# Kernel optimization log

Measured on AMD Instinct MI355X. Metric: run time of the kernel, lower is better.

The kernel has to match this reference:

```python
import jax, jax.numpy as jnp
import numpy as np

B, C, H, W = 128, 1280, 16, 16


def _conv1x1(x, w, b):
    # 1x1 conv == per-pixel linear over channels: (O,C) x (B,C,H,W) -> (B,O,H,W)
    return jnp.einsum('oc,bchw->bohw', w, x) + b[None, :, None, None]


def setup_inputs() -> dict:
    key = jax.random.key(0)
    ks = jax.random.split(key, 10)
    s = 1.0 / np.sqrt(C)
    inp = {
        'x': jax.random.normal(ks[0], (B, C, H, W), dtype=jnp.float32),
        'Wk': jax.random.uniform(ks[1], (C, C), jnp.float32, -s, s),
        'bk': jax.random.uniform(ks[2], (C,), jnp.float32, -s, s),
        'Wq': jax.random.uniform(ks[3], (C, C), jnp.float32, -s, s),
        'bq': jax.random.uniform(ks[4], (C,), jnp.float32, -s, s),
        'Wv': jax.random.uniform(ks[5], (C, C), jnp.float32, -s, s),
        'bv': jax.random.uniform(ks[6], (C,), jnp.float32, -s, s),
        'Wr': jax.random.uniform(ks[7], (C, C), jnp.float32, -s, s),
        'br': jax.random.uniform(ks[8], (C,), jnp.float32, -s, s),
        'alpha': 0.1 * jax.random.normal(ks[9], (1,), dtype=jnp.float32),
    }
    return inp


def reference(x, Wk, bk, Wq, bq, Wv, bv, Wr, br, alpha):
    b, c, h, w = x.shape
    hw = h * w
    k = _conv1x1(x, Wk, bk).reshape(b, c, hw)   # (B,C,HW)
    q = _conv1x1(x, Wq, bq).reshape(b, c, hw)   # (B,C,HW)
    v = _conv1x1(x, Wv, bv).reshape(b, c, hw)   # (B,C,HW)
    # K^T Q: (B,HW,HW) == keys.view.permute(0,2,1) @ queries.view
    scores = jnp.einsum('bcn,bcm->bnm', k, q)
    # torch.nn.Softmax2d on a 3D tensor applies softmax over dim=-3 (here: batch)
    attn = jax.nn.softmax(scores, axis=0)
    # attn @ V^T: (B,HW,HW) @ (B,HW,C) -> (B,HW,C)
    att = jnp.einsum('bnm,bmc->bnc', attn, v.transpose(0, 2, 1))
    att = att.transpose(0, 2, 1).reshape(b, c, h, w)
    out = _conv1x1(att, Wr, br)
    return alpha * out + x
```

## Files before the change

### kernel.cpp

```cpp
#include <hip/hip_runtime.h>
#include <hip/hip_bf16.h>

typedef __attribute__((ext_vector_type(8))) short bf16x8;
typedef __attribute__((ext_vector_type(4))) float f32x4;

#define GLD16(g, s) __builtin_amdgcn_global_load_lds( \
    (const __attribute__((address_space(1))) void*)(g), \
    (__attribute__((address_space(3))) void*)(s), 16, 0, 0)

#define SBAR() __builtin_amdgcn_sched_barrier(0)
#define WAIT_LGKM(n) do { asm volatile("s_waitcnt lgkmcnt(" #n ")" ::: "memory"); SBAR(); } while (0)

static constexpr int kB  = 128;
static constexpr int kC  = 1280;
static constexpr int kHW = 256;

__device__ __forceinline__ float bf2f(unsigned short u) {
    return __uint_as_float(((unsigned int)u) << 16);
}

template<int OUT_MODE, int BIAS_MODE, int ORDER>
__device__ __forceinline__ void gemm_body(
    const __hip_bfloat16* __restrict__ A,
    const __hip_bfloat16* __restrict__ Bt,
    void* __restrict__ outp,
    const float* __restrict__ bias,
    const float* __restrict__ resid,
    const float* __restrict__ alphap,
    const float* __restrict__ aux1,
    const float* __restrict__ aux2,
    int M, int N, int K,
    int ldA, int ldB, long sA, long sB, long sC, int ldC,
    char* smem, int z)
{
    const int t = threadIdx.x;
    const int w = t >> 6, l = t & 63;
    const int q = l >> 4, r16 = l & 15;
    const int wr = w >> 2, wc = w & 3;
    const int nbm = M >> 8, nbn = N >> 8;
    const int nwg = nbm * nbn;
    int f = blockIdx.x;
    {
        const int q8 = nwg >> 3, r8 = nwg & 7;
        const int xcd = f & 7, rank = f >> 3;
        f = (xcd < r8 ? xcd * (q8 + 1) : r8 * (q8 + 1) + (xcd - r8) * q8) + rank;
    }
    long m0, n0;
    if (ORDER == 0) { m0 = (long)(f % nbm) << 8; n0 = (long)(f / nbm) << 8; }
    else            { n0 = (long)(f % nbn) << 8; m0 = (long)(f / nbn) << 8; }
    const char* Azb = (const char*)(A + (long)z * sA);
    const char* Bzb = (const char*)(Bt + (long)z * sB);

    const char* pa[4];
    const char* pb[4];
    int ldsd[4];
    #pragma unroll
    for (int i = 0; i < 4; ++i) {
        const int d = i * 8192 + t * 16;
        const int row = d >> 7;
        const int cb = (d & 127) ^ ((row & 7) << 4);
        pa[i] = Azb + ((m0 + row) * (long)ldA) * 2 + cb;
        pb[i] = Bzb + ((n0 + row) * (long)ldB) * 2 + cb;
        ldsd[i] = d;
    }
    auto stage = [&](int slot) {
        char* base = smem + slot * 65536;
        #pragma unroll
        for (int i = 0; i < 4; ++i) GLD16(pa[i], base + ldsd[i]);
        #pragma unroll
        for (int i = 0; i < 4; ++i) GLD16(pb[i], base + 32768 + ldsd[i]);
        #pragma unroll
        for (int i = 0; i < 4; ++i) { pa[i] += 128; pb[i] += 128; }
    };

    const int mask = (l & 7) << 4;
    const int cx  = (q << 4) ^ mask;
    int offA[2], offB[2];
    offA[0] = (wr * 128 + r16) * 128 + cx;
    offA[1] = (wr * 128 + r16) * 128 + (cx ^ 64);
    offB[0] = 32768 + (wc * 64 + r16) * 128 + cx;
    offB[1] = 32768 + (wc * 64 + r16) * 128 + (cx ^ 64);

#define DSA(dst, bs_, mih, kk) do { const char* p_ = (bs_) + offA[kk] + (mih) * 8192; \
    dst[0] = *(const bf16x8*)(p_);        dst[1] = *(const bf16x8*)(p_ + 2048); \
    dst[2] = *(const bf16x8*)(p_ + 4096); dst[3] = *(const bf16x8*)(p_ + 6144); } while (0)
#define DSB(dst, bs_, kk) do { const char* p_ = (bs_) + offB[kk]; \
    dst[0] = *(const bf16x8*)(p_);        dst[1] = *(const bf16x8*)(p_ + 2048); \
    dst[2] = *(const bf16x8*)(p_ + 4096); dst[3] = *(const bf16x8*)(p_ + 6144); } while (0)
#define MM16(ar, br, mih) do { __builtin_amdgcn_s_setprio(1); \
    _Pragma("unroll") for (int j = 0; j < 4; ++j) \
    _Pragma("unroll") for (int ni = 0; ni < 4; ++ni) \
        acc[(mih) * 4 + j][ni] = __builtin_amdgcn_mfma_f32_16x16x32_bf16( \
            ar[j], br[ni], acc[(mih) * 4 + j][ni], 0, 0, 0); \
    __builtin_amdgcn_s_setprio(0); SBAR(); } while (0)

    f32x4 acc[8][4] = {};
    const int nK = K >> 6;
    stage(0);

    for (int tk = 0; tk < nK; ++tk) {
        const int s = tk & 1;
        asm volatile("s_waitcnt vmcnt(0)" ::: "memory");
        SBAR();
        __builtin_amdgcn_s_barrier();
        SBAR();
        if (tk + 1 < nK) stage(s ^ 1);
        SBAR();

        const char* bs_ = smem + s * 65536;
        bf16x8 aP[4], bP[4], aQ[4], bQ[4];
        DSB(bP, bs_, 0); DSA(aP, bs_, 0, 0);
        DSA(aQ, bs_, 1, 0);
        WAIT_LGKM(4);  MM16(aP, bP, 0);
        DSB(bQ, bs_, 1); DSA(aP, bs_, 0, 1);
        WAIT_LGKM(8);  MM16(aQ, bP, 1);
        DSA(aQ, bs_, 1, 1);
        WAIT_LGKM(4);  MM16(aP, bQ, 0);
        WAIT_LGKM(0);  MM16(aQ, bQ, 1);
        asm volatile("s_waitcnt lgkmcnt(0)" ::: "memory");
        SBAR();
        __builtin_amdgcn_s_barrier();
        SBAR();
    }

    const float alpha = (OUT_MODE >= 3) ? alphap[0] : 0.0f;
    #pragma unroll
    for (int mi = 0; mi < 8; ++mi) {
        #pragma unroll
        for (int ni = 0; ni < 4; ++ni) {
            #pragma unroll
            for (int r = 0; r < 4; ++r) {
                const long row = m0 + wr * 128 + mi * 16 + q * 4 + r;
                const long col = n0 + wc * 64 + ni * 16 + r16;
                float vv = acc[mi][ni][r];
                if (BIAS_MODE == 1) vv += bias[col];
                if (BIAS_MODE == 2) vv += bias[row];
                if (OUT_MODE == 0) {
                    ((__hip_bfloat16*)outp)[(long)z * sC + row * ldC + col] = __float2bfloat16(vv);
                } else if (OUT_MODE == 1) {
                    ((float*)outp)[(long)z * sC + row * ldC + col] = vv;
                } else if (OUT_MODE == 2) {
                    const long addr = (col >> 8) * (long)(kC * kHW) + row * kHW + (col & 255);
                    ((__hip_bfloat16*)outp)[addr] = __float2bfloat16(vv);
                } else if (OUT_MODE == 3) {
                    const long addr = (col >> 8) * (long)(kC * kHW) + row * kHW + (col & 255);
                    ((float*)outp)[addr] = alpha * vv + resid[addr];
                } else {
                    const long addr = (long)z * (kC * kHW) + row * kHW + col;
                    const float term = vv + aux1[row] * aux2[(long)z * 256 + col] + bias[row];
                    ((float*)outp)[addr] = alpha * term + resid[addr];
                }
            }
        }
    }
#undef DSA
#undef DSB
#undef MM16
}

template<int OUT_MODE, int BIAS_MODE, int ORDER>
__global__ __launch_bounds__(512, 2) void gemm_q(
    const __hip_bfloat16* __restrict__ A,
    const __hip_bfloat16* __restrict__ Bt,
    void* __restrict__ outp,
    const float* __restrict__ bias,
    const float* __restrict__ resid,
    const float* __restrict__ alphap,
    const float* __restrict__ aux1,
    const float* __restrict__ aux2,
    int M, int N, int K,
    int ldA, int ldB, long sA, long sB, long sC, int ldC)
{
    extern __shared__ char smem[];
    gemm_body<OUT_MODE, BIAS_MODE, ORDER>(A, Bt, outp, bias, resid, alphap,
        aux1, aux2, M, N, K, ldA, ldB, sA, sB, sC, ldC, smem, blockIdx.z);
}

__global__ __launch_bounds__(512, 2) void gemm_dual(
    const __hip_bfloat16* __restrict__ xT,
    const __hip_bfloat16* __restrict__ G,
    __hip_bfloat16* __restrict__ uT,
    const float* __restrict__ w1,
    const __hip_bfloat16* __restrict__ W2,
    __hip_bfloat16* __restrict__ rv)
{
    extern __shared__ char smem[];
    if (blockIdx.z == 0) {
        gemm_body<0, 1, 1>(xT, G, uT, w1, nullptr, nullptr, nullptr, nullptr,
            32768, 1280, 1280, 1280, 1280, 0, 0, 0, 1280, smem, 0);
    } else {
        gemm_body<2, 0, 0>(W2, xT, rv, nullptr, nullptr, nullptr, nullptr, nullptr,
            1280, 32768, 1280, 1280, 1280, 0, 0, 0, 0, smem, 0);
    }
}

__global__ __launch_bounds__(512, 2) void gemm_gsplit(
    const __hip_bfloat16* __restrict__ WkT,
    const __hip_bfloat16* __restrict__ WqT,
    const __hip_bfloat16* __restrict__ Wrb,
    const __hip_bfloat16* __restrict__ WvT,
    float* __restrict__ Gp)
{
    extern __shared__ char smem[];
    const int zz = blockIdx.z;
    const int pair = zz >> 1, ks = zz & 1;
    const __hip_bfloat16* A  = (pair ? Wrb : WkT) + ks * 640;
    const __hip_bfloat16* Bt = (pair ? WvT : WqT) + ks * 640;
    gemm_body<1, 0, 0>(A, Bt, Gp, nullptr, nullptr, nullptr, nullptr, nullptr,
        1280, 1280, 640, 1280, 1280, 0, 0, 1638400, 1280, smem, zz);
}

__global__ __launch_bounds__(256) void reduce_gw(
    const float* __restrict__ Gp,
    __hip_bfloat16* __restrict__ G, __hip_bfloat16* __restrict__ W2)
{
    const long i = ((long)blockIdx.x * 256 + threadIdx.x) * 4;
    const float4 a = *reinterpret_cast<const float4*>(Gp + i);
    const float4 b = *reinterpret_cast<const float4*>(Gp + 1638400 + i);
    G[i + 0] = __float2bfloat16(a.x + b.x);
    G[i + 1] = __float2bfloat16(a.y + b.y);
    G[i + 2] = __float2bfloat16(a.z + b.z);
    G[i + 3] = __float2bfloat16(a.w + b.w);
    const float4 c = *reinterpret_cast<const float4*>(Gp + 2L * 1638400 + i);
    const float4 d = *reinterpret_cast<const float4*>(Gp + 3L * 1638400 + i);
    W2[i + 0] = __float2bfloat16(c.x + d.x);
    W2[i + 1] = __float2bfloat16(c.y + d.y);
    W2[i + 2] = __float2bfloat16(c.z + d.z);
    W2[i + 3] = __float2bfloat16(c.w + d.w);
}

__global__ __launch_bounds__(256) void transpose_x(
    const float* __restrict__ x, __hip_bfloat16* __restrict__ xT,
    const float* __restrict__ w2, float* __restrict__ c2s)
{
    __shared__ float tile[64][65];
    __shared__ float red[4][64];
    const int b = blockIdx.z;
    const int c0 = blockIdx.x * 64;
    const int p0 = blockIdx.y * 64;
    const int tj = threadIdx.x & 63;
    const int ti = threadIdx.x >> 6;
    const float* xb = x + ((long)b * kC + c0) * kHW + p0;
    #pragma unroll
    for (int i = 0; i < 16; ++i) {
        const int c = i * 4 + ti;
        tile[c][tj] = xb[(long)c * kHW + tj];
    }
    __syncthreads();
    __hip_bfloat16* o = xT + ((long)(b * kHW + p0)) * kC + c0;
    #pragma unroll
    for (int i = 0; i < 16; ++i) {
        const int p = i * 4 + ti;
        o[(long)p * kC + tj] = __float2bfloat16(tile[tj][p]);
    }
    float s = 0.0f;
    #pragma unroll
    for (int j = 0; j < 16; ++j)
        s += tile[ti * 16 + j][tj] * w2[c0 + ti * 16 + j];
    red[ti][tj] = s;
    __syncthreads();
    if (ti == 0)
        atomicAdd(&c2s[b * 256 + p0 + tj], red[0][tj] + red[1][tj] + red[2][tj] + red[3][tj]);
}

__global__ __launch_bounds__(256) void transpose_w4(
    const float* __restrict__ Wk, __hip_bfloat16* __restrict__ WkT,
    const float* __restrict__ Wq, __hip_bfloat16* __restrict__ WqT,
    const float* __restrict__ Wv, __hip_bfloat16* __restrict__ WvT,
    const float* __restrict__ Wr, __hip_bfloat16* __restrict__ Wrb)
{
    const int zz = blockIdx.z;
    const float* W = (zz == 0) ? Wk : (zz == 1) ? Wq : (zz == 2) ? Wv : Wr;
    __hip_bfloat16* WT = (zz == 0) ? WkT : (zz == 1) ? WqT : (zz == 2) ? WvT : Wrb;
    __shared__ float tile[64][65];
    const int o0 = blockIdx.x * 64;
    const int c0 = blockIdx.y * 64;
    const int tj = threadIdx.x & 63;
    const int ti = threadIdx.x >> 6;
    #pragma unroll
    for (int i = 0; i < 16; ++i) {
        const int o = i * 4 + ti;
        tile[o][tj] = W[(long)(o0 + o) * kC + c0 + tj];
    }
    __syncthreads();
    if (zz < 3) {
        #pragma unroll
        for (int i = 0; i < 16; ++i) {
            const int c = i * 4 + ti;
            WT[(long)(c0 + c) * kC + o0 + tj] = __float2bfloat16(tile[tj][c]);
        }
    } else {
        #pragma unroll
        for (int i = 0; i < 16; ++i) {
            const int o = i * 4 + ti;
            WT[(long)(o0 + o) * kC + c0 + tj] = __float2bfloat16(tile[o][tj]);
        }
    }
}

__global__ __launch_bounds__(256) void zero_f32(float* __restrict__ p)
{
    reinterpret_cast<float4*>(p)[blockIdx.x * 256 + threadIdx.x] =
        make_float4(0.f, 0.f, 0.f, 0.f);
}

__global__ __launch_bounds__(256) void gemv_col(
    const float* __restrict__ Wk, const float* __restrict__ bq,
    const float* __restrict__ Wq, const float* __restrict__ bk,
    float* __restrict__ w1, float* __restrict__ w2)
{
    const float* W = blockIdx.y ? Wq : Wk;
    const float* v = blockIdx.y ? bk : bq;
    float* out = blockIdx.y ? w2 : w1;
    const int lj = threadIdx.x & 63;
    const int wid = threadIdx.x >> 6;
    const int c = blockIdx.x * 64 + lj;
    __shared__ float red[4][64];
    float s = 0.0f;
    for (int o = wid * 320; o < (wid + 1) * 320; ++o)
        s += W[(long)o * kC + c] * v[o];
    red[wid][lj] = s;
    __syncthreads();
    if (wid == 0) out[c] = red[0][lj] + red[1][lj] + red[2][lj] + red[3][lj];
}

__global__ __launch_bounds__(256) void gemv_row(
    const float* __restrict__ Wr, const float* __restrict__ bv, float* __restrict__ out)
{
    const int wid = threadIdx.x >> 6, lj = threadIdx.x & 63;
    const int o = blockIdx.x * 4 + wid;
    float s = 0.0f;
    #pragma unroll
    for (int j = 0; j < 20; ++j)
        s += Wr[(long)o * kC + j * 64 + lj] * bv[j * 64 + lj];
    #pragma unroll
    for (int off = 32; off > 0; off >>= 1) s += __shfl_down(s, off);
    if (lj == 0) out[o] = s;
}

__global__ __launch_bounds__(256) void dot_k(
    const float* __restrict__ a, const float* __restrict__ b, float* __restrict__ out)
{
    __shared__ float red[256];
    const int t_ = threadIdx.x;
    float s = 0.0f;
    for (int j = t_; j < kC; j += 256) s += a[j] * b[j];
    red[t_] = s; __syncthreads();
    for (int off = 128; off > 0; off >>= 1) {
        if (t_ < off) red[t_] += red[t_ + off];
        __syncthreads();
    }
    if (t_ == 0) out[0] = red[0];
}

__global__ __launch_bounds__(256) void rowsum_attn(
    const __hip_bfloat16* __restrict__ attn, float* __restrict__ rs)
{
    const int wid = threadIdx.x >> 6, lj = threadIdx.x & 63;
    const long p = (long)blockIdx.x * 4 + wid;
    const ushort4 v = *(const ushort4*)((const char*)attn + p * 512 + lj * 8);
    float s = bf2f(v.x) + bf2f(v.y) + bf2f(v.z) + bf2f(v.w);
    #pragma unroll
    for (int off = 32; off > 0; off >>= 1) s += __shfl_down(s, off);
    if (lj == 0) rs[p] = s;
}

__global__ __launch_bounds__(256) void softmax_batch(
    const float* __restrict__ sc, __hip_bfloat16* __restrict__ attn,
    const float* __restrict__ c2s, const float* __restrict__ c0p)
{
    const int pos = blockIdx.x * 256 + threadIdx.x;
    const int mcol = pos & 255;
    const float c0v = c0p[0];
    float m = -3.0e38f, s = 0.0f;
    for (int b = 0; b < kB; ++b) {
        const float v = sc[(long)b * 65536 + pos] + c2s[b * 256 + mcol] + c0v;
        const float mn = fmaxf(m, v);
        s = s * __expf(m - mn) + __expf(v - mn);
        m = mn;
    }
    const float rinv = 1.0f / s;
    for (int b = 0; b < kB; ++b) {
        const float v = sc[(long)b * 65536 + pos] + c2s[b * 256 + mcol] + c0v;
        attn[(long)b * 65536 + pos] = __float2bfloat16(__expf(v - m) * rinv);
    }
}

extern "C" void kernel_launch(void* const* d_in, const int* in_sizes, int n_in,
                              void* d_out, int out_size, void* d_ws, size_t ws_size,
                              hipStream_t stream)
{
    const float* x  = (const float*)d_in[0];
    const float* Wk = (const float*)d_in[1];
    const float* bk = (const float*)d_in[2];
    const float* Wq = (const float*)d_in[3];
    const float* bq = (const float*)d_in[4];
    const float* Wv = (const float*)d_in[5];
    const float* bv = (const float*)d_in[6];
    const float* Wr = (const float*)d_in[7];
    const float* br = (const float*)d_in[8];
    const float* al = (const float*)d_in[9];

    char* ws = (char*)d_ws;
    __hip_bfloat16* xT   = (__hip_bfloat16*)(ws);
    __hip_bfloat16* uT   = (__hip_bfloat16*)(ws + 83886080L);
    __hip_bfloat16* rv   = (__hip_bfloat16*)(ws + 167772160L);
    float*          sc   = (float*)(ws + 251658240L);
    __hip_bfloat16* attn = (__hip_bfloat16*)(ws + 285212672L);
    __hip_bfloat16* WkT  = (__hip_bfloat16*)(ws + 301989888L);
    __hip_bfloat16* Wrb  = (__hip_bfloat16*)(ws + 305266688L);
    __hip_bfloat16* WqT  = (__hip_bfloat16*)(ws + 308543488L);
    __hip_bfloat16* WvT  = (__hip_bfloat16*)(ws + 311820288L);
    __hip_bfloat16* G    = (__hip_bfloat16*)(ws + 315097088L);
    __hip_bfloat16* W2   = (__hip_bfloat16*)(ws + 318373888L);
    float*          w1   = (float*)(ws + 321650688L);
    float*          w2v  = (float*)(ws + 321655808L);
    float*          wrbv = (float*)(ws + 321660928L);
    float*          c0b  = (float*)(ws + 321666048L);
    float*          c2s  = (float*)(ws + 321666560L);
    float*          rs   = (float*)(ws + 321797632L);
    float*          Gp   = (float*)(ws + 321928704L);

    const int SMEM = 131072;
    hipFuncSetAttribute((const void*)gemm_q<1,0,0>, hipFuncAttributeMaxDynamicSharedMemorySize, SMEM);
    hipFuncSetAttribute((const void*)gemm_q<4,0,0>, hipFuncAttributeMaxDynamicSharedMemorySize, SMEM);
    hipFuncSetAttribute((const void*)gemm_dual,     hipFuncAttributeMaxDynamicSharedMemorySize, SMEM);
    hipFuncSetAttribute((const void*)gemm_gsplit,   hipFuncAttributeMaxDynamicSharedMemorySize, SMEM);

    transpose_w4<<<dim3(20, 20, 4), 256, 0, stream>>>(Wk, WkT, Wq, WqT, Wv, WvT, Wr, Wrb);
    gemv_col<<<dim3(20, 2), 256, 0, stream>>>(Wk, bq, Wq, bk, w1, w2v);
    gemv_row<<<320, 256, 0, stream>>>(Wr, bv, wrbv);
    dot_k<<<1, 256, 0, stream>>>(bk, bq, c0b);
    zero_f32<<<32, 256, 0, stream>>>(c2s);
    transpose_x<<<dim3(20, 4, 128), 256, 0, stream>>>(x, xT, w2v, c2s);

    gemm_gsplit<<<dim3(25, 1, 4), 512, SMEM, stream>>>(WkT, WqT, Wrb, WvT, Gp);
    reduce_gw<<<1600, 256, 0, stream>>>(Gp, G, W2);
    gemm_dual<<<dim3(640, 1, 2), 512, SMEM, stream>>>(xT, G, uT, w1, W2, rv);
    gemm_q<1, 0, 0><<<dim3(1, 1, 128), 512, SMEM, stream>>>(xT, uT, sc,
        nullptr, nullptr, nullptr, nullptr, nullptr,
        256, 256, 1280, 1280, 1280, 327680, 327680, 65536, 256);
    softmax_batch<<<256, 256, 0, stream>>>(sc, attn, c2s, c0b);
    rowsum_attn<<<8192, 256, 0, stream>>>(attn, rs);
    gemm_q<4, 0, 0><<<dim3(5, 1, 128), 512, SMEM, stream>>>(rv, attn, d_out,
        br, x, al, wrbv, rs,
        1280, 256, 256, 256, 256, 327680, 65536, 0, 0);
}
```

Baseline: 507.7 us.

## Split-K scores GEMM with atomics, deepen G split-K, merge small preprocessing kernels

The batched scores GEMM is split over K into two halves per batch, giving 256 blocks instead of 128, and accumulates into a pre-zeroed fp32 buffer with atomicAdd. The weight-product GEMM split-K goes from 2 to 4 slices, so it runs 200 blocks, and the reduction sums four partials. The tiny gemv and dot kernels are folded into one launch, and the zeroing of the scores buffer is combined with the c2s zeroing. This trades extra atomic traffic, a 32MB zero pass and a larger partial reduction for better CU occupancy and fewer launches. Gp now aliases the uT region, which is safe only because uT is written after reduce_gw consumes Gp.

```diff
diff --git a/kernel.cpp b/kernel.cpp
--- a/kernel.cpp
+++ b/kernel.cpp
@@ -145,10 +145,12 @@
                 } else if (OUT_MODE == 3) {
                     const long addr = (col >> 8) * (long)(kC * kHW) + row * kHW + (col & 255);
                     ((float*)outp)[addr] = alpha * vv + resid[addr];
-                } else {
+                } else if (OUT_MODE == 4) {
                     const long addr = (long)z * (kC * kHW) + row * kHW + col;
                     const float term = vv + aux1[row] * aux2[(long)z * 256 + col] + bias[row];
                     ((float*)outp)[addr] = alpha * term + resid[addr];
+                } else {
+                    atomicAdd(&((float*)outp)[(long)z * sC + row * ldC + col], vv);
                 }
             }
         }
@@ -203,11 +205,11 @@
 {
     extern __shared__ char smem[];
     const int zz = blockIdx.z;
-    const int pair = zz >> 1, ks = zz & 1;
-    const __hip_bfloat16* A  = (pair ? Wrb : WkT) + ks * 640;
-    const __hip_bfloat16* Bt = (pair ? WvT : WqT) + ks * 640;
+    const int pair = zz >> 2, kq = zz & 3;
+    const __hip_bfloat16* A  = (pair ? Wrb : WkT) + kq * 320;
+    const __hip_bfloat16* Bt = (pair ? WvT : WqT) + kq * 320;
     gemm_body<1, 0, 0>(A, Bt, Gp, nullptr, nullptr, nullptr, nullptr, nullptr,
-        1280, 1280, 640, 1280, 1280, 0, 0, 1638400, 1280, smem, zz);
+        1280, 1280, 320, 1280, 1280, 0, 0, 1638400, 1280, smem, zz);
 }
 
 __global__ __launch_bounds__(256) void reduce_gw(
@@ -215,18 +217,39 @@
     __hip_bfloat16* __restrict__ G, __hip_bfloat16* __restrict__ W2)
 {
     const long i = ((long)blockIdx.x * 256 + threadIdx.x) * 4;
-    const float4 a = *reinterpret_cast<const float4*>(Gp + i);
-    const float4 b = *reinterpret_cast<const float4*>(Gp + 1638400 + i);
-    G[i + 0] = __float2bfloat16(a.x + b.x);
-    G[i + 1] = __float2bfloat16(a.y + b.y);
-    G[i + 2] = __float2bfloat16(a.z + b.z);
-    G[i + 3] = __float2bfloat16(a.w + b.w);
-    const float4 c = *reinterpret_cast<const float4*>(Gp + 2L * 1638400 + i);
-    const float4 d = *reinterpret_cast<const float4*>(Gp + 3L * 1638400 + i);
-    W2[i + 0] = __float2bfloat16(c.x + d.x);
-    W2[i + 1] = __float2bfloat16(c.y + d.y);
-    W2[i + 2] = __float2bfloat16(c.z + d.z);
-    W2[i + 3] = __float2bfloat16(c.w + d.w);
+    float4 a = *reinterpret_cast<const float4*>(Gp + i);
+    #pragma unroll
+    for (int j = 1; j < 4; ++j) {
+        const float4 b = *reinterpret_cast<const float4*>(Gp + (long)j * 1638400 + i);
+        a.x += b.x; a.y += b.y; a.z += b.z; a.w += b.w;
+    }
+    G[i + 0] = __float2bfloat16(a.x);
+    G[i + 1] = __float2bfloat16(a.y);
+    G[i + 2] = __float2bfloat16(a.z);
+    G[i + 3] = __float2bfloat16(a.w);
+    float4 c = *reinterpret_cast<const float4*>(Gp + 4L * 1638400 + i);
+    #pragma unroll
+    for (int j = 5; j < 8; ++j) {
+        const float4 d = *reinterpret_cast<const float4*>(Gp + (long)j * 1638400 + i);
+        c.x += d.x; c.y += d.y; c.z += d.z; c.w += d.w;
+    }
+    W2[i + 0] = __float2bfloat16(c.x);
+    W2[i + 1] = __float2bfloat16(c.y);
+    W2[i + 2] = __float2bfloat16(c.z);
+    W2[i + 3] = __float2bfloat16(c.w);
+}
+
+__global__ __launch_bounds__(512, 2) void gemm_scores(
+    const __hip_bfloat16* __restrict__ xT,
+    const __hip_bfloat16* __restrict__ uT,
+    float* __restrict__ sc)
+{
+    extern __shared__ char smem[];
+    const int b = blockIdx.z >> 1, kh = blockIdx.z & 1;
+    const __hip_bfloat16* A  = xT + (long)b * 327680 + kh * 640;
+    const __hip_bfloat16* Bt = uT + (long)b * 327680 + kh * 640;
+    gemm_body<5, 0, 0>(A, Bt, sc, nullptr, nullptr, nullptr, nullptr, nullptr,
+        256, 256, 640, 1280, 1280, 0, 0, 65536, 256, smem, b);
 }
 
 __global__ __launch_bounds__(256) void transpose_x(
@@ -298,59 +321,69 @@
     }
 }
 
-__global__ __launch_bounds__(256) void zero_f32(float* __restrict__ p)
-{
-    reinterpret_cast<float4*>(p)[blockIdx.x * 256 + threadIdx.x] =
-        make_float4(0.f, 0.f, 0.f, 0.f);
-}
-
-__global__ __launch_bounds__(256) void gemv_col(
+__global__ __launch_bounds__(256) void zero_scc(
+    float* __restrict__ sc, float* __restrict__ c2s)
+{
+    const int bidx = blockIdx.x;
+    if (bidx < 8192) {
+        reinterpret_cast<float4*>(sc)[(long)bidx * 256 + threadIdx.x] =
+            make_float4(0.f, 0.f, 0.f, 0.f);
+    } else {
+        reinterpret_cast<float4*>(c2s)[(long)(bidx - 8192) * 256 + threadIdx.x] =
+            make_float4(0.f, 0.f, 0.f, 0.f);
+    }
+}
+
+__global__ __launch_bounds__(256) void preproc_small(
     const float* __restrict__ Wk, const float* __restrict__ bq,
     const float* __restrict__ Wq, const float* __restrict__ bk,
-    float* __restrict__ w1, float* __restrict__ w2)
-{
-    const float* W = blockIdx.y ? Wq : Wk;
-    const float* v = blockIdx.y ? bk : bq;
-    float* out = blockIdx.y ? w2 : w1;
-    const int lj = threadIdx.x & 63;
-    const int wid = threadIdx.x >> 6;
-    const int c = blockIdx.x * 64 + lj;
-    __shared__ float red[4][64];
-    float s = 0.0f;
-    for (int o = wid * 320; o < (wid + 1) * 320; ++o)
-        s += W[(long)o * kC + c] * v[o];
-    red[wid][lj] = s;
-    __syncthreads();
-    if (wid == 0) out[c] = red[0][lj] + red[1][lj] + red[2][lj] + red[3][lj];
-}
-
-__global__ __launch_bounds__(256) void gemv_row(
-    const float* __restrict__ Wr, const float* __restrict__ bv, float* __restrict__ out)
-{
-    const int wid = threadIdx.x >> 6, lj = threadIdx.x & 63;
-    const int o = blockIdx.x * 4 + wid;
-    float s = 0.0f;
-    #pragma unroll
-    for (int j = 0; j < 20; ++j)
-        s += Wr[(long)o * kC + j * 64 + lj] * bv[j * 64 + lj];
-    #pragma unroll
-    for (int off = 32; off > 0; off >>= 1) s += __shfl_down(s, off);
-    if (lj == 0) out[o] = s;
-}
-
-__global__ __launch_bounds__(256) void dot_k(
-    const float* __restrict__ a, const float* __restrict__ b, float* __restrict__ out)
-{
-    __shared__ float red[256];
-    const int t_ = threadIdx.x;
-    float s = 0.0f;
-    for (int j = t_; j < kC; j += 256) s += a[j] * b[j];
-    red[t_] = s; __syncthreads();
-    for (int off = 128; off > 0; off >>= 1) {
-        if (t_ < off) red[t_] += red[t_ + off];
+    const float* __restrict__ Wr, const float* __restrict__ bv,
+    float* __restrict__ w1, float* __restrict__ w2,
+    float* __restrict__ wrbv, float* __restrict__ c0out)
+{
+    const int bidx = blockIdx.x;
+    if (bidx < 40) {
+        const int y = bidx >> 5 | ((bidx & 31) >= 20 ? 1 : 0);
+    }
+    if (bidx < 40) {
+        const int y = bidx / 20;
+        const int bx = bidx % 20;
+        const float* W = y ? Wq : Wk;
+        const float* v = y ? bk : bq;
+        float* out = y ? w2 : w1;
+        const int lj = threadIdx.x & 63;
+        const int wid = threadIdx.x >> 6;
+        const int c = bx * 64 + lj;
+        __shared__ float red[4][64];
+        float s = 0.0f;
+        for (int o = wid * 320; o < (wid + 1) * 320; ++o)
+            s += W[(long)o * kC + c] * v[o];
+        red[wid][lj] = s;
         __syncthreads();
-    }
-    if (t_ == 0) out[0] = red[0];
+        if (wid == 0) out[c] = red[0][lj] + red[1][lj] + red[2][lj] + red[3][lj];
+    } else if (bidx < 360) {
+        const int bx = bidx - 40;
+        const int wid = threadIdx.x >> 6, lj = threadIdx.x & 63;
+        const int o = bx * 4 + wid;
+        float s = 0.0f;
+        #pragma unroll
+        for (int j = 0; j < 20; ++j)
+            s += Wr[(long)o * kC + j * 64 + lj] * bv[j * 64 + lj];
+        #pragma unroll
+        for (int off = 32; off > 0; off >>= 1) s += __shfl_down(s, off);
+        if (lj == 0) wrbv[o] = s;
+    } else {
+        __shared__ float red[256];
+        const int t_ = threadIdx.x;
+        float s = 0.0f;
+        for (int j = t_; j < kC; j += 256) s += bk[j] * bq[j];
+        red[t_] = s; __syncthreads();
+        for (int off = 128; off > 0; off >>= 1) {
+            if (t_ < off) red[t_] += red[t_ + off];
+            __syncthreads();
+        }
+        if (t_ == 0) c0out[0] = red[0];
+    }
 }
 
 __global__ __launch_bounds__(256) void rowsum_attn(
@@ -404,6 +437,7 @@
     char* ws = (char*)d_ws;
     __hip_bfloat16* xT   = (__hip_bfloat16*)(ws);
     __hip_bfloat16* uT   = (__hip_bfloat16*)(ws + 83886080L);
+    float*          Gp   = (float*)(ws + 83886080L);
     __hip_bfloat16* rv   = (__hip_bfloat16*)(ws + 167772160L);
     float*          sc   = (float*)(ws + 251658240L);
     __hip_bfloat16* attn = (__hip_bfloat16*)(ws + 285212672L);
@@ -419,27 +453,22 @@
     float*          c0b  = (float*)(ws + 321666048L);
     float*          c2s  = (float*)(ws + 321666560L);
     float*          rs   = (float*)(ws + 321797632L);
-    float*          Gp   = (float*)(ws + 321928704L);
 
     const int SMEM = 131072;
-    hipFuncSetAttribute((const void*)gemm_q<1,0,0>, hipFuncAttributeMaxDynamicSharedMemorySize, SMEM);
     hipFuncSetAttribute((const void*)gemm_q<4,0,0>, hipFuncAttributeMaxDynamicSharedMemorySize, SMEM);
-    hipFuncSetAttribute((const void*)gemm_dual,     hipFuncAttributeMaxDynamicSharedMemorySize, SMEM);
-    hipFuncSetAttribute((const void*)gemm_gsplit,   hipFuncAttributeMaxDynamicSharedMemorySize, SMEM);
+    hipFuncSetAttribute((const void*)gemm_dual,   hipFuncAttributeMaxDynamicSharedMemorySize, SMEM);
+    hipFuncSetAttribute((const void*)gemm_gsplit, hipFuncAttributeMaxDynamicSharedMemorySize, SMEM);
+    hipFuncSetAttribute((const void*)gemm_scores, hipFuncAttributeMaxDynamicSharedMemorySize, SMEM);
 
     transpose_w4<<<dim3(20, 20, 4), 256, 0, stream>>>(Wk, WkT, Wq, WqT, Wv, WvT, Wr, Wrb);
-    gemv_col<<<dim3(20, 2), 256, 0, stream>>>(Wk, bq, Wq, bk, w1, w2v);
-    gemv_row<<<320, 256, 0, stream>>>(Wr, bv, wrbv);
-    dot_k<<<1, 256, 0, stream>>>(bk, bq, c0b);
-    zero_f32<<<32, 256, 0, stream>>>(c2s);
+    preproc_small<<<361, 256, 0, stream>>>(Wk, bq, Wq, bk, Wr, bv, w1, w2v, wrbv, c0b);
+    zero_scc<<<8224, 256, 0, stream>>>(sc, c2s);
     transpose_x<<<dim3(20, 4, 128), 256, 0, stream>>>(x, xT, w2v, c2s);
 
-    gemm_gsplit<<<dim3(25, 1, 4), 512, SMEM, stream>>>(WkT, WqT, Wrb, WvT, Gp);
+    gemm_gsplit<<<dim3(25, 1, 8), 512, SMEM, stream>>>(WkT, WqT, Wrb, WvT, Gp);
     reduce_gw<<<1600, 256, 0, stream>>>(Gp, G, W2);
     gemm_dual<<<dim3(640, 1, 2), 512, SMEM, stream>>>(xT, G, uT, w1, W2, rv);
-    gemm_q<1, 0, 0><<<dim3(1, 1, 128), 512, SMEM, stream>>>(xT, uT, sc,
-        nullptr, nullptr, nullptr, nullptr, nullptr,
-        256, 256, 1280, 1280, 1280, 327680, 327680, 65536, 256);
+    gemm_scores<<<dim3(1, 1, 256), 512, SMEM, stream>>>(xT, uT, sc);
     softmax_batch<<<256, 256, 0, stream>>>(sc, attn, c2s, c0b);
     rowsum_attn<<<8192, 256, 0, stream>>>(attn, rs);
     gemm_q<4, 0, 0><<<dim3(5, 1, 128), 512, SMEM, stream>>>(rv, attn, d_out,
```

New measurement: 533.1 us. 1.05x slower.

## Split scores GEMM over K halves and merge small preprocessing kernels

Applied to the files above, without the earlier changes.

The per-batch scores GEMM, which launched only 128 workgroups, is split into two K-halves, giving 256 workgroups. The two partial score buffers are summed inside the batch-softmax kernel. The three tiny GEMV/dot kernels are fused into one launch to cut launch overhead, and workspace buffers are re-aliased to make room for the second partial scores buffer. The split doubles fp32 score writes and adds extra reads in the softmax.

```diff
diff --git a/kernel.cpp b/kernel.cpp
--- a/kernel.cpp
+++ b/kernel.cpp
@@ -229,6 +229,20 @@
     W2[i + 3] = __float2bfloat16(c.w + d.w);
 }
 
+__global__ __launch_bounds__(512, 2) void gemm_scores(
+    const __hip_bfloat16* __restrict__ xT,
+    const __hip_bfloat16* __restrict__ uT,
+    float* __restrict__ sc)
+{
+    extern __shared__ char smem[];
+    const int b = blockIdx.z >> 1, kh = blockIdx.z & 1;
+    const __hip_bfloat16* A  = xT + (long)b * 327680 + kh * 640;
+    const __hip_bfloat16* Bt = uT + (long)b * 327680 + kh * 640;
+    float* out = sc + (long)kh * 8388608;
+    gemm_body<1, 0, 0>(A, Bt, out, nullptr, nullptr, nullptr, nullptr, nullptr,
+        256, 256, 640, 1280, 1280, 0, 0, 65536, 256, smem, b);
+}
+
 __global__ __launch_bounds__(256) void transpose_x(
     const float* __restrict__ x, __hip_bfloat16* __restrict__ xT,
     const float* __restrict__ w2, float* __restrict__ c2s)
@@ -304,53 +318,53 @@
         make_float4(0.f, 0.f, 0.f, 0.f);
 }
 
-__global__ __launch_bounds__(256) void gemv_col(
+__global__ __launch_bounds__(256) void preproc_small(
     const float* __restrict__ Wk, const float* __restrict__ bq,
     const float* __restrict__ Wq, const float* __restrict__ bk,
-    float* __restrict__ w1, float* __restrict__ w2)
-{
-    const float* W = blockIdx.y ? Wq : Wk;
-    const float* v = blockIdx.y ? bk : bq;
-    float* out = blockIdx.y ? w2 : w1;
-    const int lj = threadIdx.x & 63;
-    const int wid = threadIdx.x >> 6;
-    const int c = blockIdx.x * 64 + lj;
-    __shared__ float red[4][64];
-    float s = 0.0f;
-    for (int o = wid * 320; o < (wid + 1) * 320; ++o)
-        s += W[(long)o * kC + c] * v[o];
-    red[wid][lj] = s;
-    __syncthreads();
-    if (wid == 0) out[c] = red[0][lj] + red[1][lj] + red[2][lj] + red[3][lj];
-}
-
-__global__ __launch_bounds__(256) void gemv_row(
-    const float* __restrict__ Wr, const float* __restrict__ bv, float* __restrict__ out)
-{
-    const int wid = threadIdx.x >> 6, lj = threadIdx.x & 63;
-    const int o = blockIdx.x * 4 + wid;
-    float s = 0.0f;
-    #pragma unroll
-    for (int j = 0; j < 20; ++j)
-        s += Wr[(long)o * kC + j * 64 + lj] * bv[j * 64 + lj];
-    #pragma unroll
-    for (int off = 32; off > 0; off >>= 1) s += __shfl_down(s, off);
-    if (lj == 0) out[o] = s;
-}
-
-__global__ __launch_bounds__(256) void dot_k(
-    const float* __restrict__ a, const float* __restrict__ b, float* __restrict__ out)
-{
-    __shared__ float red[256];
-    const int t_ = threadIdx.x;
-    float s = 0.0f;
-    for (int j = t_; j < kC; j += 256) s += a[j] * b[j];
-    red[t_] = s; __syncthreads();
-    for (int off = 128; off > 0; off >>= 1) {
-        if (t_ < off) red[t_] += red[t_ + off];
+    const float* __restrict__ Wr, const float* __restrict__ bv,
+    float* __restrict__ w1, float* __restrict__ w2,
+    float* __restrict__ wrbv, float* __restrict__ c0out)
+{
+    const int bidx = blockIdx.x;
+    if (bidx < 40) {
+        const int y = bidx / 20;
+        const int bx = bidx % 20;
+        const float* W = y ? Wq : Wk;
+        const float* v = y ? bk : bq;
+        float* out = y ? w2 : w1;
+        const int lj = threadIdx.x & 63;
+        const int wid = threadIdx.x >> 6;
+        const int c = bx * 64 + lj;
+        __shared__ float red[4][64];
+        float s = 0.0f;
+        for (int o = wid * 320; o < (wid + 1) * 320; ++o)
+            s += W[(long)o * kC + c] * v[o];
+        red[wid][lj] = s;
         __syncthreads();
-    }
-    if (t_ == 0) out[0] = red[0];
+        if (wid == 0) out[c] = red[0][lj] + red[1][lj] + red[2][lj] + red[3][lj];
+    } else if (bidx < 360) {
+        const int bx = bidx - 40;
+        const int wid = threadIdx.x >> 6, lj = threadIdx.x & 63;
+        const int o = bx * 4 + wid;
+        float s = 0.0f;
+        #pragma unroll
+        for (int j = 0; j < 20; ++j)
+            s += Wr[(long)o * kC + j * 64 + lj] * bv[j * 64 + lj];
+        #pragma unroll
+        for (int off = 32; off > 0; off >>= 1) s += __shfl_down(s, off);
+        if (lj == 0) wrbv[o] = s;
+    } else {
+        __shared__ float red[256];
+        const int t_ = threadIdx.x;
+        float s = 0.0f;
+        for (int j = t_; j < kC; j += 256) s += bk[j] * bq[j];
+        red[t_] = s; __syncthreads();
+        for (int off = 128; off > 0; off >>= 1) {
+            if (t_ < off) red[t_] += red[t_ + off];
+            __syncthreads();
+        }
+        if (t_ == 0) c0out[0] = red[0];
+    }
 }
 
 __global__ __launch_bounds__(256) void rowsum_attn(
@@ -372,17 +386,20 @@
     const int pos = blockIdx.x * 256 + threadIdx.x;
     const int mcol = pos & 255;
     const float c0v = c0p[0];
+    const float* sc1 = sc + 8388608;
     float m = -3.0e38f, s = 0.0f;
     for (int b = 0; b < kB; ++b) {
-        const float v = sc[(long)b * 65536 + pos] + c2s[b * 256 + mcol] + c0v;
+        const long i = (long)b * 65536 + pos;
+        const float v = sc[i] + sc1[i] + c2s[b * 256 + mcol] + c0v;
         const float mn = fmaxf(m, v);
         s = s * __expf(m - mn) + __expf(v - mn);
         m = mn;
     }
     const float rinv = 1.0f / s;
     for (int b = 0; b < kB; ++b) {
-        const float v = sc[(long)b * 65536 + pos] + c2s[b * 256 + mcol] + c0v;
-        attn[(long)b * 65536 + pos] = __float2bfloat16(__expf(v - m) * rinv);
+        const long i = (long)b * 65536 + pos;
+        const float v = sc[i] + sc1[i] + c2s[b * 256 + mcol] + c0v;
+        attn[i] = __float2bfloat16(__expf(v - m) * rinv);
     }
 }
 
@@ -404,42 +421,38 @@
     char* ws = (char*)d_ws;
     __hip_bfloat16* xT   = (__hip_bfloat16*)(ws);
     __hip_bfloat16* uT   = (__hip_bfloat16*)(ws + 83886080L);
+    __hip_bfloat16* attn = (__hip_bfloat16*)(ws + 83886080L);
     __hip_bfloat16* rv   = (__hip_bfloat16*)(ws + 167772160L);
+    float*          Gp   = (float*)(ws + 167772160L);
     float*          sc   = (float*)(ws + 251658240L);
-    __hip_bfloat16* attn = (__hip_bfloat16*)(ws + 285212672L);
-    __hip_bfloat16* WkT  = (__hip_bfloat16*)(ws + 301989888L);
-    __hip_bfloat16* Wrb  = (__hip_bfloat16*)(ws + 305266688L);
-    __hip_bfloat16* WqT  = (__hip_bfloat16*)(ws + 308543488L);
-    __hip_bfloat16* WvT  = (__hip_bfloat16*)(ws + 311820288L);
-    __hip_bfloat16* G    = (__hip_bfloat16*)(ws + 315097088L);
-    __hip_bfloat16* W2   = (__hip_bfloat16*)(ws + 318373888L);
-    float*          w1   = (float*)(ws + 321650688L);
-    float*          w2v  = (float*)(ws + 321655808L);
-    float*          wrbv = (float*)(ws + 321660928L);
-    float*          c0b  = (float*)(ws + 321666048L);
-    float*          c2s  = (float*)(ws + 321666560L);
-    float*          rs   = (float*)(ws + 321797632L);
-    float*          Gp   = (float*)(ws + 321928704L);
+    __hip_bfloat16* WkT  = (__hip_bfloat16*)(ws + 318767104L);
+    __hip_bfloat16* Wrb  = (__hip_bfloat16*)(ws + 322043904L);
+    __hip_bfloat16* WqT  = (__hip_bfloat16*)(ws + 325320704L);
+    __hip_bfloat16* WvT  = (__hip_bfloat16*)(ws + 328597504L);
+    __hip_bfloat16* G    = (__hip_bfloat16*)(ws + 331874304L);
+    __hip_bfloat16* W2   = (__hip_bfloat16*)(ws + 335151104L);
+    float*          w1   = (float*)(ws + 338427904L);
+    float*          w2v  = (float*)(ws + 338433024L);
+    float*          wrbv = (float*)(ws + 338438144L);
+    float*          c0b  = (float*)(ws + 338443264L);
+    float*          c2s  = (float*)(ws + 338443776L);
+    float*          rs   = (float*)(ws + 338574848L);
 
     const int SMEM = 131072;
-    hipFuncSetAttribute((const void*)gemm_q<1,0,0>, hipFuncAttributeMaxDynamicSharedMemorySize, SMEM);
     hipFuncSetAttribute((const void*)gemm_q<4,0,0>, hipFuncAttributeMaxDynamicSharedMemorySize, SMEM);
-    hipFuncSetAttribute((const void*)gemm_dual,     hipFuncAttributeMaxDynamicSharedMemorySize, SMEM);
-    hipFuncSetAttribute((const void*)gemm_gsplit,   hipFuncAttributeMaxDynamicSharedMemorySize, SMEM);
+    hipFuncSetAttribute((const void*)gemm_dual,   hipFuncAttributeMaxDynamicSharedMemorySize, SMEM);
+    hipFuncSetAttribute((const void*)gemm_gsplit, hipFuncAttributeMaxDynamicSharedMemorySize, SMEM);
+    hipFuncSetAttribute((const void*)gemm_scores, hipFuncAttributeMaxDynamicSharedMemorySize, SMEM);
 
     transpose_w4<<<dim3(20, 20, 4), 256, 0, stream>>>(Wk, WkT, Wq, WqT, Wv, WvT, Wr, Wrb);
-    gemv_col<<<dim3(20, 2), 256, 0, stream>>>(Wk, bq, Wq, bk, w1, w2v);
-    gemv_row<<<320, 256, 0, stream>>>(Wr, bv, wrbv);
-    dot_k<<<1, 256, 0, stream>>>(bk, bq, c0b);
+    preproc_small<<<361, 256, 0, stream>>>(Wk, bq, Wq, bk, Wr, bv, w1, w2v, wrbv, c0b);
     zero_f32<<<32, 256, 0, stream>>>(c2s);
     transpose_x<<<dim3(20, 4, 128), 256, 0, stream>>>(x, xT, w2v, c2s);
 
     gemm_gsplit<<<dim3(25, 1, 4), 512, SMEM, stream>>>(WkT, WqT, Wrb, WvT, Gp);
     reduce_gw<<<1600, 256, 0, stream>>>(Gp, G, W2);
     gemm_dual<<<dim3(640, 1, 2), 512, SMEM, stream>>>(xT, G, uT, w1, W2, rv);
-    gemm_q<1, 0, 0><<<dim3(1, 1, 128), 512, SMEM, stream>>>(xT, uT, sc,
-        nullptr, nullptr, nullptr, nullptr, nullptr,
-        256, 256, 1280, 1280, 1280, 327680, 327680, 65536, 256);
+    gemm_scores<<<dim3(1, 1, 256), 512, SMEM, stream>>>(xT, uT, sc);
     softmax_batch<<<256, 256, 0, stream>>>(sc, attn, c2s, c0b);
     rowsum_attn<<<8192, 256, 0, stream>>>(attn, rs);
     gemm_q<4, 0, 0><<<dim3(5, 1, 128), 512, SMEM, stream>>>(rv, attn, d_out,
```

After: 491.4 us. 1.03x faster.
